# Performance work log

Measured on AMD Instinct MI355X. Metric: run time of the kernel, lower is better.

## Reference

```python
import jax, jax.numpy as jnp
import numpy as np
import math

N_NODES = 50000
N_EDGES = 800000
HIDDEN = 128
NUM_GAUSS = 50
NUM_FILTERS = 128
CUTOFF = 10.0
SHIFT = math.log(2.0)


def setup_inputs() -> dict:
    key = jax.random.key(0)
    ks = jax.random.split(key, 12)
    x = jax.random.normal(ks[0], (N_NODES, HIDDEN), dtype=jnp.float32)
    edge_index = jax.random.randint(ks[1], (2, N_EDGES), 0, N_NODES, dtype=jnp.int64)
    edge_weight = jax.random.uniform(ks[2], (N_EDGES,), dtype=jnp.float32)
    edge_attr = jax.random.normal(ks[3], (N_EDGES, NUM_GAUSS), dtype=jnp.float32)
    # learned parameters (xavier-ish scale)
    def xavier(k, shape):
        fan_in, fan_out = shape[1], shape[0]
        bound = math.sqrt(6.0 / (fan_in + fan_out))
        return jax.random.uniform(k, shape, dtype=jnp.float32, minval=-bound, maxval=bound)
    mlp_w1 = xavier(ks[4], (NUM_FILTERS, NUM_GAUSS))
    mlp_b1 = jnp.zeros((NUM_FILTERS,), jnp.float32)
    mlp_w2 = xavier(ks[5], (NUM_FILTERS, NUM_FILTERS))
    mlp_b2 = jnp.zeros((NUM_FILTERS,), jnp.float32)
    lin1_w = xavier(ks[6], (NUM_FILTERS, HIDDEN))   # no bias
    lin2_w = xavier(ks[7], (HIDDEN, NUM_FILTERS))
    lin2_b = jnp.zeros((HIDDEN,), jnp.float32)
    lin_w = xavier(ks[8], (HIDDEN, HIDDEN))
    lin_b = jnp.zeros((HIDDEN,), jnp.float32)
    return {"x": x, "edge_index": edge_index, "edge_weight": edge_weight,
            "edge_attr": edge_attr, "mlp_w1": mlp_w1, "mlp_b1": mlp_b1,
            "mlp_w2": mlp_w2, "mlp_b2": mlp_b2, "lin1_w": lin1_w,
            "lin2_w": lin2_w, "lin2_b": lin2_b, "lin_w": lin_w, "lin_b": lin_b}


def shifted_softplus(v):
    return jax.nn.softplus(v) - SHIFT


def reference(x, edge_index, edge_weight, edge_attr, mlp_w1, mlp_b1,
              mlp_w2, mlp_b2, lin1_w, lin2_w, lin2_b, lin_w, lin_b):
    src, dst = edge_index[0], edge_index[1]
    # cosine cutoff per edge: [E]
    C = 0.5 * (jnp.cos(edge_weight * (jnp.pi / CUTOFF)) + 1.0)
    # edge filter MLP: [E, num_filters]
    h_e = shifted_softplus(edge_attr @ mlp_w1.T + mlp_b1)
    W = (h_e @ mlp_w2.T + mlp_b2) * C[:, None]
    # node projection, gather-multiply-scatter aggregation
    h = x @ lin1_w.T                       # [N, num_filters]
    msg = h[src] * W                       # [E, num_filters]
    agg = jax.ops.segment_sum(msg, dst, num_segments=N_NODES)  # [N, num_filters]
    h = agg @ lin2_w.T + lin2_b            # [N, hidden]
    h = shifted_softplus(h)
    out = h @ lin_w.T + lin_b              # [N, hidden]
    return out
```

## Files before the change

### kernel.cpp

```cpp
#include <hip/hip_runtime.h>
#include <hip/hip_bf16.h>
#include <math.h>

#define E_NUM 800000
#define NN 50000
#define NG 50
#define NTW (E_NUM / 16)
#define EDGE_BLOCKS 768

typedef __bf16 bf16x8 __attribute__((ext_vector_type(8)));
typedef float f32x4 __attribute__((ext_vector_type(4)));
typedef unsigned short ushortx8 __attribute__((ext_vector_type(8)));

__device__ __forceinline__ unsigned short f2b(float f) {
  union { __bf16 h; unsigned short u; } v; v.h = (__bf16)f; return v.u;
}
__device__ __forceinline__ float b2f(unsigned short u) {
  union { unsigned u; float f; } v; v.u = ((unsigned)u) << 16; return v.f;
}
__device__ __forceinline__ float sspf(float v) {
  float e = __builtin_amdgcn_exp2f(-1.4426950408889634f * fabsf(v));
  return fmaxf(v, 0.f) + 0.6931471805599453f * __builtin_amdgcn_logf(fmaf(0.5f, e, 0.5f));
}

__global__ __launch_bounds__(256) void k_hist(const int* __restrict__ ei, int* __restrict__ counts) {
  int e = blockIdx.x * 256 + threadIdx.x;
  if (e < E_NUM) atomicAdd(&counts[ei[E_NUM + e]], 1);
}

__global__ __launch_bounds__(1024) void k_scan(const int* __restrict__ counts,
                                               int* __restrict__ cursor) {
  __shared__ int tot[1024];
  const int t = threadIdx.x;
  const int C = (NN + 1023) >> 10;
  int lo = t * C, hi = lo + C; if (hi > NN) hi = NN; if (lo > NN) lo = NN;
  int s = 0;
  for (int i = lo; i < hi; ++i) s += counts[i];
  tot[t] = s;
  __syncthreads();
  int mine = s;
  for (int o = 1; o < 1024; o <<= 1) {
    int v = (t >= o) ? tot[t - o] : 0;
    __syncthreads();
    tot[t] += v;
    __syncthreads();
  }
  int run = tot[t] - mine;
  for (int i = lo; i < hi; ++i) { int c = counts[i]; cursor[i] = run; run += c; }
}

__global__ __launch_bounds__(256) void k_scatter2(
    const int* __restrict__ ei, const float* __restrict__ ew,
    const float* __restrict__ attr, int* __restrict__ cursor,
    int* __restrict__ srcS, int* __restrict__ dstS,
    float* __restrict__ cS, unsigned short* __restrict__ attrS)
{
  int e = blockIdx.x * 256 + threadIdx.x;
  if (e >= E_NUM) return;
  int d = ei[E_NUM + e];
  int pos = atomicAdd(&cursor[d], 1);
  srcS[pos] = ei[e];
  dstS[pos] = d;
  cS[pos] = 0.5f * (__builtin_amdgcn_cosf(ew[e] * 0.05f) + 1.f);
  const float* rp = attr + (long)e * NG;
  unsigned short* op = attrS + (long)pos * 64;
  float2 v[25];
#pragma unroll
  for (int i = 0; i < 25; ++i) v[i] = *(const float2*)(rp + 2 * i);
#pragma unroll
  for (int c = 0; c < 8; ++c) {
    ushortx8 o;
#pragma unroll
    for (int j = 0; j < 8; ++j) {
      int k = c * 8 + j;
      o[j] = (k < NG) ? f2b((k & 1) ? v[k >> 1].y : v[k >> 1].x) : (unsigned short)0;
    }
    *(ushortx8*)(op + c * 8) = o;
  }
}

__global__ __launch_bounds__(256) void k_mfma_gemm(
    const float* __restrict__ X, const float* __restrict__ Wm,
    const float* __restrict__ bias, float* __restrict__ out, int act, int nrows)
{
  __shared__ __attribute__((aligned(16))) unsigned short s_x[128 * 128];
  __shared__ __attribute__((aligned(16))) unsigned short s_w[128 * 128];
  const int tid = threadIdx.x;
  const int w = tid >> 6, lane = tid & 63, q = lane >> 4, n16 = lane & 15;
  const int base = blockIdx.x * 128;

  for (int c = tid; c < 128 * 16; c += 256) {
    int f = c >> 4, ch = c & 15;
    const float4* wp = (const float4*)(Wm + f * 128 + ch * 8);
    float4 v0 = wp[0], v1 = wp[1];
    ushortx8 v = { f2b(v0.x), f2b(v0.y), f2b(v0.z), f2b(v0.w),
                   f2b(v1.x), f2b(v1.y), f2b(v1.z), f2b(v1.w) };
    *(ushortx8*)&s_w[(f << 7) + ((ch ^ (f & 15)) << 3)] = v;
  }
  for (int c = tid; c < 128 * 16; c += 256) {
    int r = c >> 4, ch = c & 15;
    int n = base + r;
    float4 v0 = {0.f, 0.f, 0.f, 0.f}, v1 = v0;
    if (n < nrows) {
      const float4* xp = (const float4*)(X + (long)n * 128 + ch * 8);
      v0 = xp[0]; v1 = xp[1];
    }
    ushortx8 v = { f2b(v0.x), f2b(v0.y), f2b(v0.z), f2b(v0.w),
                   f2b(v1.x), f2b(v1.y), f2b(v1.z), f2b(v1.w) };
    *(ushortx8*)&s_x[(r << 7) + ((ch ^ (r & 15)) << 3)] = v;
  }
  __syncthreads();

  float bv[8];
#pragma unroll
  for (int t = 0; t < 8; ++t) bv[t] = bias ? bias[t * 16 + n16] : 0.f;

  bf16x8 a[2][4];
#pragma unroll
  for (int g = 0; g < 2; ++g) {
    int r = w * 32 + g * 16 + n16;
#pragma unroll
    for (int ks = 0; ks < 4; ++ks)
      a[g][ks] = *(const bf16x8*)&s_x[(r << 7) + (((ks * 4 + q) ^ (r & 15)) << 3)];
  }
#pragma unroll
  for (int t = 0; t < 8; ++t) {
    int f = t * 16 + n16;
    bf16x8 b[4];
#pragma unroll
    for (int ks = 0; ks < 4; ++ks)
      b[ks] = *(const bf16x8*)&s_w[(f << 7) + (((ks * 4 + q) ^ (f & 15)) << 3)];
#pragma unroll
    for (int g = 0; g < 2; ++g) {
      f32x4 acc = {0.f, 0.f, 0.f, 0.f};
#pragma unroll
      for (int ks = 0; ks < 4; ++ks)
        acc = __builtin_amdgcn_mfma_f32_16x16x32_bf16(a[g][ks], b[ks], acc, 0, 0, 0);
#pragma unroll
      for (int r = 0; r < 4; ++r) {
        int n = base + w * 32 + g * 16 + q * 4 + r;
        if (n < nrows) {
          float v = acc[r] + bv[t];
          if (act) v = sspf(v);
          out[(long)n * 128 + f] = v;
        }
      }
    }
  }
}

__global__ __launch_bounds__(256, 2) void k_gemm23(
    const float* __restrict__ A, const float* __restrict__ W2,
    const float* __restrict__ B2, const float* __restrict__ W3,
    const float* __restrict__ B3, float* __restrict__ out, int nrows)
{
  __shared__ __attribute__((aligned(16))) unsigned short s_x[128 * 128];
  __shared__ __attribute__((aligned(16))) unsigned short s_w[128 * 128];
  const int tid = threadIdx.x;
  const int w = tid >> 6, lane = tid & 63, q = lane >> 4, n16 = lane & 15;
  const int base = blockIdx.x * 128;

  for (int c = tid; c < 128 * 16; c += 256) {
    int f = c >> 4, ch = c & 15;
    const float4* wp = (const float4*)(W2 + f * 128 + ch * 8);
    float4 v0 = wp[0], v1 = wp[1];
    ushortx8 v = { f2b(v0.x), f2b(v0.y), f2b(v0.z), f2b(v0.w),
                   f2b(v1.x), f2b(v1.y), f2b(v1.z), f2b(v1.w) };
    *(ushortx8*)&s_w[(f << 7) + ((ch ^ (f & 15)) << 3)] = v;
  }
  for (int c = tid; c < 128 * 16; c += 256) {
    int r = c >> 4, ch = c & 15;
    int n = base + r;
    float4 v0 = {0.f, 0.f, 0.f, 0.f}, v1 = v0;
    if (n < nrows) {
      const float4* xp = (const float4*)(A + (long)n * 128 + ch * 8);
      v0 = xp[0]; v1 = xp[1];
    }
    ushortx8 v = { f2b(v0.x), f2b(v0.y), f2b(v0.z), f2b(v0.w),
                   f2b(v1.x), f2b(v1.y), f2b(v1.z), f2b(v1.w) };
    *(ushortx8*)&s_x[(r << 7) + ((ch ^ (r & 15)) << 3)] = v;
  }
  __syncthreads();

  float b2v[8], b3v[8];
#pragma unroll
  for (int t = 0; t < 8; ++t) { b2v[t] = B2[t * 16 + n16]; b3v[t] = B3[t * 16 + n16]; }

  bf16x8 a[2][4];
#pragma unroll
  for (int g = 0; g < 2; ++g) {
    int r = w * 32 + g * 16 + n16;
#pragma unroll
    for (int ks = 0; ks < 4; ++ks)
      a[g][ks] = *(const bf16x8*)&s_x[(r << 7) + (((ks * 4 + q) ^ (r & 15)) << 3)];
  }
  float acc1[8][2][4];
#pragma unroll
  for (int t = 0; t < 8; ++t) {
    int f = t * 16 + n16;
    bf16x8 b[4];
#pragma unroll
    for (int ks = 0; ks < 4; ++ks)
      b[ks] = *(const bf16x8*)&s_w[(f << 7) + (((ks * 4 + q) ^ (f & 15)) << 3)];
#pragma unroll
    for (int g = 0; g < 2; ++g) {
      f32x4 acc = {0.f, 0.f, 0.f, 0.f};
#pragma unroll
      for (int ks = 0; ks < 4; ++ks)
        acc = __builtin_amdgcn_mfma_f32_16x16x32_bf16(a[g][ks], b[ks], acc, 0, 0, 0);
#pragma unroll
      for (int r = 0; r < 4; ++r) acc1[t][g][r] = acc[r];
    }
  }
  __syncthreads();

#pragma unroll
  for (int t = 0; t < 8; ++t) {
    int f = t * 16 + n16;
#pragma unroll
    for (int g = 0; g < 2; ++g)
#pragma unroll
      for (int r = 0; r < 4; ++r) {
        int row = w * 32 + g * 16 + q * 4 + r;
        s_x[(row << 7) + (((f >> 3) ^ (row & 15)) << 3) + (f & 7)] =
            f2b(sspf(acc1[t][g][r] + b2v[t]));
      }
  }
  for (int c = tid; c < 128 * 16; c += 256) {
    int f = c >> 4, ch = c & 15;
    const float4* wp = (const float4*)(W3 + f * 128 + ch * 8);
    float4 v0 = wp[0], v1 = wp[1];
    ushortx8 v = { f2b(v0.x), f2b(v0.y), f2b(v0.z), f2b(v0.w),
                   f2b(v1.x), f2b(v1.y), f2b(v1.z), f2b(v1.w) };
    *(ushortx8*)&s_w[(f << 7) + ((ch ^ (f & 15)) << 3)] = v;
  }
  __syncthreads();

#pragma unroll
  for (int g = 0; g < 2; ++g) {
    int r = w * 32 + g * 16 + n16;
#pragma unroll
    for (int ks = 0; ks < 4; ++ks)
      a[g][ks] = *(const bf16x8*)&s_x[(r << 7) + (((ks * 4 + q) ^ (r & 15)) << 3)];
  }
#pragma unroll
  for (int t = 0; t < 8; ++t) {
    int f = t * 16 + n16;
    bf16x8 b[4];
#pragma unroll
    for (int ks = 0; ks < 4; ++ks)
      b[ks] = *(const bf16x8*)&s_w[(f << 7) + (((ks * 4 + q) ^ (f & 15)) << 3)];
#pragma unroll
    for (int g = 0; g < 2; ++g) {
      f32x4 acc = {0.f, 0.f, 0.f, 0.f};
#pragma unroll
      for (int ks = 0; ks < 4; ++ks)
        acc = __builtin_amdgcn_mfma_f32_16x16x32_bf16(a[g][ks], b[ks], acc, 0, 0, 0);
#pragma unroll
      for (int r = 0; r < 4; ++r) {
        int n = base + w * 32 + g * 16 + q * 4 + r;
        if (n < nrows) out[(long)n * 128 + f] = acc[r] + b3v[t];
      }
    }
  }
}

__global__ __launch_bounds__(256, 3) void k_edge_agg(
    const float* __restrict__ attr, const int* __restrict__ ei,
    const float* __restrict__ ew, const float* __restrict__ w1,
    const float* __restrict__ b1, const float* __restrict__ w2,
    const float* __restrict__ b2, const float* __restrict__ h,
    const int* __restrict__ srcS, const int* __restrict__ dstS,
    const float* __restrict__ cS, const unsigned short* __restrict__ attrS,
    float* __restrict__ agg, int mode)
{
  __shared__ __attribute__((aligned(16))) unsigned short s_w2[128 * 128];
  __shared__ __attribute__((aligned(16))) unsigned short s_scr[4 * 16 * 136];

  const int tid  = threadIdx.x;
  const int w    = tid >> 6;
  const int lane = tid & 63;
  const int q    = lane >> 4;
  const int n16  = lane & 15;

  for (int i = tid; i < 128 * 128; i += 256) {
    int f = i >> 7, k = i & 127;
    int pos = (f << 7) + ((((k >> 3) ^ (f & 15)) << 3)) + (k & 7);
    s_w2[pos] = f2b(w2[i]);
  }
  bf16x8 w1A[8], w1B[8];
#pragma unroll
  for (int t = 0; t < 8; ++t) {
    int f = t * 16 + n16;
    const float* row = w1 + f * NG;
    union { ushortx8 u; bf16x8 b; } ua, ub;
#pragma unroll
    for (int j = 0; j < 8; ++j) ua.u[j] = f2b(row[q * 8 + j]);
#pragma unroll
    for (int j = 0; j < 8; ++j) { int k = 32 + q * 8 + j; ub.u[j] = (k < NG) ? f2b(row[k]) : (unsigned short)0; }
    w1A[t] = ua.b; w1B[t] = ub.b;
  }
  float b1v[8], b2v[8];
#pragma unroll
  for (int t = 0; t < 8; ++t) {
    b1v[t] = b1[t * 16 + n16];
    b2v[t] = b2[t * 16 + n16];
  }
  __syncthreads();

  unsigned short* scr = s_scr + w * (16 * 136);
  const int nwaves = EDGE_BLOCKS * 4;
  const int gw = blockIdx.x * 4 + w;

  if (mode == 1) {
    int tile = gw;
    bf16x8 uaC, ubC;
    int svs[16];
    {
      const long e0 = (long)tile * 16;
      uaC = *(const bf16x8*)(attrS + (e0 + n16) * 64 + q * 8);
      ubC = *(const bf16x8*)(attrS + (e0 + n16) * 64 + 32 + q * 8);
#pragma unroll
      for (int i = 0; i < 16; ++i) svs[i] = __builtin_amdgcn_readfirstlane(srcS[e0 + i]);
    }

    for (; tile < NTW; tile += nwaves) {
      const int e0 = tile * 16;
      const int tn = tile + nwaves;
      const bool hasnext = (tn < NTW);

      float2 hv[16];
#pragma unroll
      for (int i = 0; i < 16; ++i)
        hv[i] = *(const float2*)(h + (long)svs[i] * 128 + (lane << 1));
      float cvv[4];
#pragma unroll
      for (int r = 0; r < 4; ++r) cvv[r] = cS[e0 + q * 4 + r];
      bf16x8 uaN = uaC, ubN = ubC;
      int svN[16];
#pragma unroll
      for (int i = 0; i < 16; ++i) svN[i] = 0;
      if (hasnext) {
        const long en = (long)tn * 16;
        uaN = *(const bf16x8*)(attrS + (en + n16) * 64 + q * 8);
        ubN = *(const bf16x8*)(attrS + (en + n16) * 64 + 32 + q * 8);
#pragma unroll
        for (int i = 0; i < 16; ++i) svN[i] = srcS[en + i];
      }

#pragma unroll
      for (int t = 0; t < 8; ++t) {
        f32x4 acc = {0.f, 0.f, 0.f, 0.f};
        acc = __builtin_amdgcn_mfma_f32_16x16x32_bf16(uaC, w1A[t], acc, 0, 0, 0);
        acc = __builtin_amdgcn_mfma_f32_16x16x32_bf16(ubC, w1B[t], acc, 0, 0, 0);
        int f = t * 16 + n16;
#pragma unroll
        for (int r = 0; r < 4; ++r) {
          int row = q * 4 + r;
          scr[row * 136 + f] = f2b(sspf(acc[r] + b1v[t]));
        }
      }
      __builtin_amdgcn_wave_barrier();

      bf16x8 a2f[4];
#pragma unroll
      for (int ks = 0; ks < 4; ++ks)
        a2f[ks] = *(const bf16x8*)&scr[n16 * 136 + ks * 32 + q * 8];
      __builtin_amdgcn_wave_barrier();

#pragma unroll
      for (int t = 0; t < 8; ++t) {
        int f = t * 16 + n16;
        f32x4 acc = {0.f, 0.f, 0.f, 0.f};
#pragma unroll
        for (int ks = 0; ks < 4; ++ks) {
          bf16x8 bb = *(const bf16x8*)&s_w2[(f << 7) + (((ks * 4 + q) ^ (f & 15)) << 3)];
          acc = __builtin_amdgcn_mfma_f32_16x16x32_bf16(a2f[ks], bb, acc, 0, 0, 0);
        }
#pragma unroll
        for (int r = 0; r < 4; ++r) {
          int row = q * 4 + r;
          scr[row * 136 + f] = f2b((acc[r] + b2v[t]) * cvv[r]);
        }
      }
      __builtin_amdgcn_wave_barrier();

      int dvv[16];
#pragma unroll
      for (int i = 0; i < 16; ++i) dvv[i] = dstS[e0 + i];
      int dcur = -1, rowstart = 0;
      float ax = 0.f, ay = 0.f;
#pragma unroll
      for (int i = 0; i < 16; ++i) {
        int dv = __builtin_amdgcn_readfirstlane(dvv[i]);
        if (dv != dcur) {
          if (dcur >= 0) {
            float* ap = agg + (long)dcur * 128 + (lane << 1);
            if (rowstart == 0) { atomicAdd(ap, ax); atomicAdd(ap + 1, ay); }
            else { float2 o; o.x = ax; o.y = ay; *(float2*)ap = o; }
          }
          dcur = dv; ax = 0.f; ay = 0.f; rowstart = i;
        }
        unsigned wp = *(const unsigned*)&scr[i * 136 + (lane << 1)];
        ax = fmaf(hv[i].x, b2f((unsigned short)(wp & 0xffffu)), ax);
        ay = fmaf(hv[i].y, b2f((unsigned short)(wp >> 16)), ay);
      }
      {
        float* ap = agg + (long)dcur * 128 + (lane << 1);
        atomicAdd(ap, ax); atomicAdd(ap + 1, ay);
      }
      __builtin_amdgcn_wave_barrier();

      if (hasnext) {
#pragma unroll
        for (int i = 0; i < 16; ++i) svs[i] = __builtin_amdgcn_readfirstlane(svN[i]);
        uaC = uaN; ubC = ubN;
      }
    }
  } else {
    for (int tile = gw; tile < NTW; tile += nwaves) {
      const int e0 = tile * 16;
      const int er = e0 + n16;
      const float* rp = attr + (long)er * NG;

      float2 p0 = *(const float2*)(rp + q * 8);
      float2 p1 = *(const float2*)(rp + q * 8 + 2);
      float2 p2 = *(const float2*)(rp + q * 8 + 4);
      float2 p3 = *(const float2*)(rp + q * 8 + 6);
      float2 p4 = {0.f, 0.f}, p5 = {0.f, 0.f}, p6 = {0.f, 0.f}, p7 = {0.f, 0.f};
      if (q < 2) {
        const float* rp2 = rp + 32 + q * 8;
        p4 = *(const float2*)(rp2);
        p5 = *(const float2*)(rp2 + 2);
        p6 = *(const float2*)(rp2 + 4);
        p7 = *(const float2*)(rp2 + 6);
      } else if (q == 2) {
        p4 = *(const float2*)(rp + 48);
      }
      union { ushortx8 u; bf16x8 b; } ua, ub;
      ua.u[0] = f2b(p0.x); ua.u[1] = f2b(p0.y); ua.u[2] = f2b(p1.x); ua.u[3] = f2b(p1.y);
      ua.u[4] = f2b(p2.x); ua.u[5] = f2b(p2.y); ua.u[6] = f2b(p3.x); ua.u[7] = f2b(p3.y);
      ub.u[0] = f2b(p4.x); ub.u[1] = f2b(p4.y); ub.u[2] = f2b(p5.x); ub.u[3] = f2b(p5.y);
      ub.u[4] = f2b(p6.x); ub.u[5] = f2b(p6.y); ub.u[6] = f2b(p7.x); ub.u[7] = f2b(p7.y);

#pragma unroll
      for (int t = 0; t < 8; ++t) {
        f32x4 acc = {0.f, 0.f, 0.f, 0.f};
        acc = __builtin_amdgcn_mfma_f32_16x16x32_bf16(ua.b, w1A[t], acc, 0, 0, 0);
        acc = __builtin_amdgcn_mfma_f32_16x16x32_bf16(ub.b, w1B[t], acc, 0, 0, 0);
        int f = t * 16 + n16;
#pragma unroll
        for (int r = 0; r < 4; ++r) {
          int row = q * 4 + r;
          scr[row * 136 + f] = f2b(sspf(acc[r] + b1v[t]));
        }
      }
      __builtin_amdgcn_wave_barrier();

      bf16x8 a2f[4];
#pragma unroll
      for (int ks = 0; ks < 4; ++ks)
        a2f[ks] = *(const bf16x8*)&scr[n16 * 136 + ks * 32 + q * 8];
      __builtin_amdgcn_wave_barrier();

      float cvv[4];
      int srcv[4], dstv[4];
#pragma unroll
      for (int r = 0; r < 4; ++r) {
        cvv[r] = 0.5f * (__builtin_amdgcn_cosf(ew[e0 + q * 4 + r] * 0.05f) + 1.f);
        srcv[r] = ei[e0 + q * 4 + r];
        dstv[r] = ei[E_NUM + e0 + q * 4 + r];
      }

#pragma unroll
      for (int t = 0; t < 8; ++t) {
        int f = t * 16 + n16;
        f32x4 acc = {0.f, 0.f, 0.f, 0.f};
#pragma unroll
        for (int ks = 0; ks < 4; ++ks) {
          bf16x8 bb = *(const bf16x8*)&s_w2[(f << 7) + (((ks * 4 + q) ^ (f & 15)) << 3)];
          acc = __builtin_amdgcn_mfma_f32_16x16x32_bf16(a2f[ks], bb, acc, 0, 0, 0);
        }
#pragma unroll
        for (int r = 0; r < 4; ++r) {
          float msg = h[(long)srcv[r] * 128 + f] * (acc[r] + b2v[t]) * cvv[r];
          atomicAdd(&agg[(long)dstv[r] * 128 + f], msg);
        }
      }
      __builtin_amdgcn_wave_barrier();
    }
  }
}

extern "C" void kernel_launch(void* const* d_in, const int* in_sizes, int n_in,
                              void* d_out, int out_size, void* d_ws, size_t ws_size,
                              hipStream_t stream) {
  const float* x     = (const float*)d_in[0];
  const int*   ei    = (const int*)  d_in[1];
  const float* ew    = (const float*)d_in[2];
  const float* attr  = (const float*)d_in[3];
  const float* w1    = (const float*)d_in[4];
  const float* b1    = (const float*)d_in[5];
  const float* w2    = (const float*)d_in[6];
  const float* b2    = (const float*)d_in[7];
  const float* lin1w = (const float*)d_in[8];
  const float* lin2w = (const float*)d_in[9];
  const float* lin2b = (const float*)d_in[10];
  const float* linw  = (const float*)d_in[11];
  const float* linb  = (const float*)d_in[12];
  float* out = (float*)d_out;

  char* base = (char*)d_ws;
  float* agg    = (float*)base;
  float* h      = agg + (size_t)NN * 128;
  int*   counts = (int*)(h + (size_t)NN * 128);
  int*   cursor = counts + NN;
  int*   srcS   = cursor + NN;
  int*   dstS   = srcS + E_NUM;
  float* cS     = (float*)(dstS + E_NUM);
  size_t head   = (size_t)((char*)(cS + E_NUM) - base);
  size_t aoff   = (head + 255) & ~(size_t)255;
  unsigned short* attrS = (unsigned short*)(base + aoff);
  size_t need   = aoff + (size_t)E_NUM * 64 * sizeof(unsigned short);
  const int mode = (ws_size >= need) ? 1 : 0;

  const int gemm_grid = (NN + 127) / 128;
  (void)hipMemsetAsync(agg, 0, (size_t)NN * 128 * sizeof(float), stream);
  if (mode == 1) {
    (void)hipMemsetAsync(counts, 0, (size_t)NN * sizeof(int), stream);
    k_hist<<<(E_NUM + 255) / 256, 256, 0, stream>>>(ei, counts);
    k_scan<<<1, 1024, 0, stream>>>(counts, cursor);
    k_scatter2<<<(E_NUM + 255) / 256, 256, 0, stream>>>(ei, ew, attr, cursor,
                                                        srcS, dstS, cS, attrS);
  }
  k_mfma_gemm<<<gemm_grid, 256, 0, stream>>>(x, lin1w, nullptr, h, 0, NN);
  k_edge_agg<<<EDGE_BLOCKS, 256, 0, stream>>>(attr, ei, ew, w1, b1, w2, b2, h,
                                              srcS, dstS, cS, attrS, agg, mode);
  k_gemm23<<<gemm_grid, 256, 0, stream>>>(agg, lin2w, lin2b, linw, linb, out, NN);
}
```

Baseline: 711.9 us.

## Use 512-thread edge blocks and shrink the per-wave prefetch register footprint

The edge-aggregation kernel now launches 512-thread blocks with a higher occupancy hint, and shares the bf16 W2 copy in LDS across eight waves instead of four. The deep software prefetch of the 16 gathered h rows and source indices is dropped. Those gathers now happen just before the scatter, in two halves of eight, and only the attr fragment is prefetched, issued mid-tile. This is meant to cut VGPR pressure so more waves can hide gather latency, at the cost of exposing the h-gather latency inside each tile.

```diff
diff --git a/kernel.cpp b/kernel.cpp
--- a/kernel.cpp
+++ b/kernel.cpp
@@ -6,7 +6,7 @@
 #define NN 50000
 #define NG 50
 #define NTW (E_NUM / 16)
-#define EDGE_BLOCKS 768
+#define EDGE_BLOCKS 512
 
 typedef __bf16 bf16x8 __attribute__((ext_vector_type(8)));
 typedef float f32x4 __attribute__((ext_vector_type(4)));
@@ -265,7 +265,7 @@
   }
 }
 
-__global__ __launch_bounds__(256, 3) void k_edge_agg(
+__global__ __launch_bounds__(512, 4) void k_edge_agg(
     const float* __restrict__ attr, const int* __restrict__ ei,
     const float* __restrict__ ew, const float* __restrict__ w1,
     const float* __restrict__ b1, const float* __restrict__ w2,
@@ -275,7 +275,7 @@
     float* __restrict__ agg, int mode)
 {
   __shared__ __attribute__((aligned(16))) unsigned short s_w2[128 * 128];
-  __shared__ __attribute__((aligned(16))) unsigned short s_scr[4 * 16 * 136];
+  __shared__ __attribute__((aligned(16))) unsigned short s_scr[8 * 16 * 136];
 
   const int tid  = threadIdx.x;
   const int w    = tid >> 6;
@@ -283,7 +283,7 @@
   const int q    = lane >> 4;
   const int n16  = lane & 15;
 
-  for (int i = tid; i < 128 * 128; i += 256) {
+  for (int i = tid; i < 128 * 128; i += 512) {
     int f = i >> 7, k = i & 127;
     int pos = (f << 7) + ((((k >> 3) ^ (f & 15)) << 3)) + (k & 7);
     s_w2[pos] = f2b(w2[i]);
@@ -309,44 +309,20 @@
   __syncthreads();
 
   unsigned short* scr = s_scr + w * (16 * 136);
-  const int nwaves = EDGE_BLOCKS * 4;
-  const int gw = blockIdx.x * 4 + w;
+  const int nwaves = EDGE_BLOCKS * 8;
+  const int gw = blockIdx.x * 8 + w;
 
   if (mode == 1) {
-    int tile = gw;
-    bf16x8 uaC, ubC;
-    int svs[16];
+    bf16x8 uaN, ubN;
     {
-      const long e0 = (long)tile * 16;
-      uaC = *(const bf16x8*)(attrS + (e0 + n16) * 64 + q * 8);
-      ubC = *(const bf16x8*)(attrS + (e0 + n16) * 64 + 32 + q * 8);
-#pragma unroll
-      for (int i = 0; i < 16; ++i) svs[i] = __builtin_amdgcn_readfirstlane(srcS[e0 + i]);
-    }
-
-    for (; tile < NTW; tile += nwaves) {
+      const long e0 = (long)gw * 16;
+      uaN = *(const bf16x8*)(attrS + (e0 + n16) * 64 + q * 8);
+      ubN = *(const bf16x8*)(attrS + (e0 + n16) * 64 + 32 + q * 8);
+    }
+
+    for (int tile = gw; tile < NTW; tile += nwaves) {
       const int e0 = tile * 16;
-      const int tn = tile + nwaves;
-      const bool hasnext = (tn < NTW);
-
-      float2 hv[16];
-#pragma unroll
-      for (int i = 0; i < 16; ++i)
-        hv[i] = *(const float2*)(h + (long)svs[i] * 128 + (lane << 1));
-      float cvv[4];
-#pragma unroll
-      for (int r = 0; r < 4; ++r) cvv[r] = cS[e0 + q * 4 + r];
-      bf16x8 uaN = uaC, ubN = ubC;
-      int svN[16];
-#pragma unroll
-      for (int i = 0; i < 16; ++i) svN[i] = 0;
-      if (hasnext) {
-        const long en = (long)tn * 16;
-        uaN = *(const bf16x8*)(attrS + (en + n16) * 64 + q * 8);
-        ubN = *(const bf16x8*)(attrS + (en + n16) * 64 + 32 + q * 8);
-#pragma unroll
-        for (int i = 0; i < 16; ++i) svN[i] = srcS[en + i];
-      }
+      bf16x8 uaC = uaN, ubC = ubN;
 
 #pragma unroll
       for (int t = 0; t < 8; ++t) {
@@ -368,6 +344,19 @@
         a2f[ks] = *(const bf16x8*)&scr[n16 * 136 + ks * 32 + q * 8];
       __builtin_amdgcn_wave_barrier();
 
+      {
+        const int tn = tile + nwaves;
+        if (tn < NTW) {
+          const long en = (long)tn * 16;
+          uaN = *(const bf16x8*)(attrS + (en + n16) * 64 + q * 8);
+          ubN = *(const bf16x8*)(attrS + (en + n16) * 64 + 32 + q * 8);
+        }
+      }
+
+      float cvv[4];
+#pragma unroll
+      for (int r = 0; r < 4; ++r) cvv[r] = cS[e0 + q * 4 + r];
+
 #pragma unroll
       for (int t = 0; t < 8; ++t) {
         int f = t * 16 + n16;
@@ -385,37 +374,39 @@
       }
       __builtin_amdgcn_wave_barrier();
 
-      int dvv[16];
-#pragma unroll
-      for (int i = 0; i < 16; ++i) dvv[i] = dstS[e0 + i];
       int dcur = -1, rowstart = 0;
       float ax = 0.f, ay = 0.f;
 #pragma unroll
-      for (int i = 0; i < 16; ++i) {
-        int dv = __builtin_amdgcn_readfirstlane(dvv[i]);
-        if (dv != dcur) {
-          if (dcur >= 0) {
-            float* ap = agg + (long)dcur * 128 + (lane << 1);
-            if (rowstart == 0) { atomicAdd(ap, ax); atomicAdd(ap + 1, ay); }
-            else { float2 o; o.x = ax; o.y = ay; *(float2*)ap = o; }
+      for (int hf = 0; hf < 2; ++hf) {
+        int dv[8]; float2 hv[8];
+#pragma unroll
+        for (int i = 0; i < 8; ++i) {
+          int pos = e0 + hf * 8 + i;
+          dv[i] = __builtin_amdgcn_readfirstlane(dstS[pos]);
+          int sv = __builtin_amdgcn_readfirstlane(srcS[pos]);
+          hv[i] = *(const float2*)(h + (long)sv * 128 + (lane << 1));
+        }
+#pragma unroll
+        for (int i = 0; i < 8; ++i) {
+          int row = hf * 8 + i;
+          if (dv[i] != dcur) {
+            if (dcur >= 0) {
+              float* ap = agg + (long)dcur * 128 + (lane << 1);
+              if (rowstart == 0) { atomicAdd(ap, ax); atomicAdd(ap + 1, ay); }
+              else { float2 o; o.x = ax; o.y = ay; *(float2*)ap = o; }
+            }
+            dcur = dv[i]; ax = 0.f; ay = 0.f; rowstart = row;
           }
-          dcur = dv; ax = 0.f; ay = 0.f; rowstart = i;
-        }
-        unsigned wp = *(const unsigned*)&scr[i * 136 + (lane << 1)];
-        ax = fmaf(hv[i].x, b2f((unsigned short)(wp & 0xffffu)), ax);
-        ay = fmaf(hv[i].y, b2f((unsigned short)(wp >> 16)), ay);
+          unsigned wp = *(const unsigned*)&scr[row * 136 + (lane << 1)];
+          ax = fmaf(hv[i].x, b2f((unsigned short)(wp & 0xffffu)), ax);
+          ay = fmaf(hv[i].y, b2f((unsigned short)(wp >> 16)), ay);
+        }
       }
       {
         float* ap = agg + (long)dcur * 128 + (lane << 1);
         atomicAdd(ap, ax); atomicAdd(ap + 1, ay);
       }
       __builtin_amdgcn_wave_barrier();
-
-      if (hasnext) {
-#pragma unroll
-        for (int i = 0; i < 16; ++i) svs[i] = __builtin_amdgcn_readfirstlane(svN[i]);
-        uaC = uaN; ubC = ubN;
-      }
     }
   } else {
     for (int tile = gw; tile < NTW; tile += nwaves) {
@@ -534,7 +525,7 @@
                                                         srcS, dstS, cS, attrS);
   }
   k_mfma_gemm<<<gemm_grid, 256, 0, stream>>>(x, lin1w, nullptr, h, 0, NN);
-  k_edge_agg<<<EDGE_BLOCKS, 256, 0, stream>>>(attr, ei, ew, w1, b1, w2, b2, h,
+  k_edge_agg<<<EDGE_BLOCKS, 512, 0, stream>>>(attr, ei, ew, w1, b1, w2, b2, h,
                                               srcS, dstS, cS, attrS, agg, mode);
   k_gemm23<<<gemm_grid, 256, 0, stream>>>(agg, lin2w, lin2b, linw, linb, out, NN);
 }
```

Result: faster. 611.5 us (-14.1%).
